# Kernel optimization log

Measured on AMD Instinct MI355X. Metric: run time of the kernel, lower is better.

Reference implementation:

```python
import jax, jax.numpy as jnp
import numpy as np

N = 50000   # nodes
E = 800000  # edges (avg degree 16)
D = 128     # in = hidden = out feats


def setup_inputs() -> dict:
    key = jax.random.key(0)
    ks = jax.random.split(key, 9)
    x = jax.random.normal(ks[0], (N, D), dtype=jnp.float32)
    edge_index = jax.random.randint(ks[1], (2, E), 0, N, dtype=jnp.int64)
    s = 1.0 / np.sqrt(D)
    # SAGEConv layer 0 (128 -> 128): lin_l (aggregated neighbors, with bias), lin_r (root, no bias)
    Wl0 = jax.random.uniform(ks[2], (D, D), jnp.float32, -s, s)
    Wr0 = jax.random.uniform(ks[3], (D, D), jnp.float32, -s, s)
    b0 = jax.random.uniform(ks[4], (D,), jnp.float32, -s, s)
    # SAGEConv layer 1 (128 -> 128)
    Wl1 = jax.random.uniform(ks[5], (D, D), jnp.float32, -s, s)
    Wr1 = jax.random.uniform(ks[6], (D, D), jnp.float32, -s, s)
    b1 = jax.random.uniform(ks[7], (D,), jnp.float32, -s, s)
    return {"x": x, "edge_index": edge_index,
            "Wl0": Wl0, "Wr0": Wr0, "b0": b0,
            "Wl1": Wl1, "Wr1": Wr1, "b1": b1}


def _sage_conv(x, src, dst, Wl, Wr, b):
    # mean aggregation of neighbor messages x[src] into dst nodes
    msgs = x[src]                                                    # [E, D]
    summed = jax.ops.segment_sum(msgs, dst, num_segments=N)         # [N, D]
    deg = jax.ops.segment_sum(jnp.ones((src.shape[0], 1), x.dtype), dst,
                              num_segments=N)                       # [N, 1]
    agg = summed / jnp.maximum(deg, 1.0)
    # out = lin_l(agg) + lin_r(x); only lin_l has bias (PyG default)
    return agg @ Wl.T + b + x @ Wr.T


def reference(x, edge_index, Wl0, Wr0, b0, Wl1, Wr1, b1):
    src, dst = edge_index[0], edge_index[1]
    h = jax.nn.relu(_sage_conv(x, src, dst, Wl0, Wr0, b0))
    out = _sage_conv(h, src, dst, Wl1, Wr1, b1)  # no ReLU on last layer
    return out
```

## Files before the change

### kernel.cpp

```cpp
#include <hip/hip_runtime.h>


#define D 128
#define NBITS 7
#define BNODES 128
#define GA 64
typedef unsigned short u16;
typedef unsigned u32;
typedef short bf16x8 __attribute__((ext_vector_type(8)));
typedef float f32x4 __attribute__((ext_vector_type(4)));

__device__ __forceinline__ u16 f2bf(float f) {
    union { float f; unsigned u; } x;
    x.f = f;
    unsigned r = x.u + 0x7FFF + ((x.u >> 16) & 1);
    return (u16)(r >> 16);
}
__device__ __forceinline__ float bf2f(u16 b) {
    union { unsigned u; float f; } x;
    x.u = ((unsigned)b) << 16;
    return x.f;
}


__global__ __launch_bounds__(1024) void bucket_hist(const int* __restrict__ dst,
                                                    int* __restrict__ Gcounts,
                                                    int E, int NB, int chunk) {
    __shared__ int cnt[512];
    for (int i = threadIdx.x; i < NB; i += 1024) cnt[i] = 0;
    __syncthreads();
    int base = blockIdx.x * chunk;
    int end = base + chunk; if (end > E) end = E;
    for (int e = base + threadIdx.x; e < end; e += 1024)
        atomicAdd(&cnt[dst[e] >> NBITS], 1);
    __syncthreads();
    for (int b = threadIdx.x; b < NB; b += 1024)
        Gcounts[b * GA + blockIdx.x] = cnt[b];
}

__global__ __launch_bounds__(1024) void scan1_kernel(const int* __restrict__ in,
                                                     int* __restrict__ excl,
                                                     int* __restrict__ totals, int n) {
    int chunk = blockIdx.x;
    int i = chunk * 1024 + threadIdx.x;
    int v = (i < n) ? in[i] : 0;
    int lane = threadIdx.x & 63;
    int wid = threadIdx.x >> 6;
    int s = v;
    #pragma unroll
    for (int off = 1; off < 64; off <<= 1) {
        int t = __shfl_up(s, off);
        if (lane >= off) s += t;
    }
    __shared__ int wsum[16];
    if (lane == 63) wsum[wid] = s;
    __syncthreads();
    if (wid == 0) {
        int ws = (lane < 16) ? wsum[lane] : 0;
        #pragma unroll
        for (int off = 1; off < 16; off <<= 1) {
            int t = __shfl_up(ws, off);
            if (lane >= off) ws += t;
        }
        if (lane < 16) wsum[lane] = ws;
    }
    __syncthreads();
    int wave_off = (wid > 0) ? wsum[wid - 1] : 0;
    int incl = s + wave_off;
    if (i < n) excl[i] = incl - v;
    if (threadIdx.x == 1023) totals[chunk] = incl;
}

__global__ __launch_bounds__(1024) void scan_add(int* __restrict__ Sc,
                                                 const int* __restrict__ totals, int n) {
    int chunk = blockIdx.x;
    int i = chunk * 1024 + threadIdx.x;
    int off = 0;
    for (int j = 0; j < chunk; ++j) off += totals[j];
    if (i < n) Sc[i] += off;
}

__global__ __launch_bounds__(1024) void bucket_scatter(const int* __restrict__ src,
                                                       const int* __restrict__ dst,
                                                       const int* __restrict__ Sc,
                                                       u32* __restrict__ Ebuck,
                                                       int E, int NB, int chunk) {
    __shared__ int cur[512];
    for (int b = threadIdx.x; b < NB; b += 1024) cur[b] = Sc[b * GA + blockIdx.x];
    __syncthreads();
    int base = blockIdx.x * chunk;
    int end = base + chunk; if (end > E) end = E;
    for (int e = base + threadIdx.x; e < end; e += 1024) {
        int d = dst[e];
        int b = d >> NBITS;
        int pos = atomicAdd(&cur[b], 1);
        Ebuck[pos] = ((u32)(d & (BNODES - 1)) << 16) | (u32)src[e];
    }
}

__global__ __launch_bounds__(256) void bucket_sort_csr(u32* __restrict__ Ebuck,
                                                       const int* __restrict__ Sc,
                                                       int* __restrict__ row_ptr,
                                                       int E, int N, int NB) {
    __shared__ int hist[BNODES], excl[BNODES], cur[BNODES];
    __shared__ u16 sorted[8192];
    int b = blockIdx.x;
    int start = Sc[b * GA];
    int endv = (b + 1 < NB) ? Sc[(b + 1) * GA] : E;
    int cnt = endv - start;
    if (cnt > 8192) cnt = 8192;
    for (int i = threadIdx.x; i < BNODES; i += 256) hist[i] = 0;
    __syncthreads();
    for (int i = threadIdx.x; i < cnt; i += 256)
        atomicAdd(&hist[Ebuck[start + i] >> 16], 1);
    __syncthreads();
    if (threadIdx.x == 0) {
        int run = 0;
        for (int i = 0; i < BNODES; ++i) { excl[i] = run; run += hist[i]; }
    }
    __syncthreads();
    for (int i = threadIdx.x; i < BNODES; i += 256) {
        cur[i] = excl[i];
        int g = b * BNODES + i;
        if (g <= N) row_ptr[g] = start + excl[i];
    }
    __syncthreads();
    for (int i = threadIdx.x; i < cnt; i += 256) {
        u32 r = Ebuck[start + i];
        int pos = atomicAdd(&cur[r >> 16], 1);
        sorted[pos] = (u16)(r & 0xFFFF);
    }
    __syncthreads();
    for (int i = threadIdx.x; i < cnt; i += 256)
        ((int*)Ebuck)[start + i] = (int)sorted[i];
}

__global__ void f32_to_bf16_kernel(const float* __restrict__ in, u16* __restrict__ out, int n4) {
    int i = blockIdx.x * 256 + threadIdx.x;
    if (i < n4) {
        float4 v = *(const float4*)&in[i * 4];
        ushort4 o;
        o.x = f2bf(v.x); o.y = f2bf(v.y); o.z = f2bf(v.z); o.w = f2bf(v.w);
        *(ushort4*)&out[i * 4] = o;
    }
}

__global__ void convert_weights(const float* __restrict__ w0, const float* __restrict__ w1,
                                const float* __restrict__ w2, const float* __restrict__ w3,
                                u16* __restrict__ o0, u16* __restrict__ o1,
                                u16* __restrict__ o2, u16* __restrict__ o3) {
    int i = blockIdx.x * 256 + threadIdx.x;
    const int q = D * D / 4;
    int m = i / q, j = i % q;
    const float* in = (m == 0) ? w0 : (m == 1) ? w1 : (m == 2) ? w2 : w3;
    u16* out = (m == 0) ? o0 : (m == 1) ? o1 : (m == 2) ? o2 : o3;
    float4 v = *(const float4*)&in[j * 4];
    ushort4 o;
    o.x = f2bf(v.x); o.y = f2bf(v.y); o.z = f2bf(v.z); o.w = f2bf(v.w);
    *(ushort4*)&out[j * 4] = o;
}

__global__ __launch_bounds__(256) void aggregate_bf16(const u16* __restrict__ xb,
                                                      const int* __restrict__ row_ptr,
                                                      const int* __restrict__ csr,
                                                      u16* __restrict__ aggb, int n) {
    int node = blockIdx.x * 4 + (threadIdx.x >> 6);
    if (node >= n) return;
    int lane = threadIdx.x & 63;
    int half = lane >> 5;
    int fl = (lane & 31) * 4;
    int begin = row_ptr[node], end = row_ptr[node + 1];
    float a0 = 0.f, a1 = 0.f, a2 = 0.f, a3 = 0.f;
    int j = begin + half;
    for (; j + 2 < end; j += 4) {
        int s0 = csr[j], s1 = csr[j + 2];
        ushort4 v0 = *(const ushort4*)&xb[s0 * D + fl];
        ushort4 v1 = *(const ushort4*)&xb[s1 * D + fl];
        a0 += bf2f(v0.x) + bf2f(v1.x);
        a1 += bf2f(v0.y) + bf2f(v1.y);
        a2 += bf2f(v0.z) + bf2f(v1.z);
        a3 += bf2f(v0.w) + bf2f(v1.w);
    }
    if (j < end) {
        int s0 = csr[j];
        ushort4 v0 = *(const ushort4*)&xb[s0 * D + fl];
        a0 += bf2f(v0.x); a1 += bf2f(v0.y); a2 += bf2f(v0.z); a3 += bf2f(v0.w);
    }
    a0 += __shfl_xor(a0, 32);
    a1 += __shfl_xor(a1, 32);
    a2 += __shfl_xor(a2, 32);
    a3 += __shfl_xor(a3, 32);
    if (half == 0) {
        int d = end - begin;
        if (d < 1) d = 1;
        float inv = 1.0f / (float)d;
        ushort4 o;
        o.x = f2bf(a0 * inv); o.y = f2bf(a1 * inv);
        o.z = f2bf(a2 * inv); o.w = f2bf(a3 * inv);
        *(ushort4*)&aggb[node * D + fl] = o;
    }
}

#define LSTR 136

__global__ __launch_bounds__(256) void gemm_mfma(const u16* __restrict__ Aroot,
                                                 const u16* __restrict__ Wr,
                                                 const u16* __restrict__ Agg,
                                                 const u16* __restrict__ Wl,
                                                 const float* __restrict__ bias,
                                                 void* __restrict__ out,
                                                 int n, int mode) {
    __shared__ __align__(16) u16 Lr[64 * LSTR];
    __shared__ __align__(16) u16 Lg[64 * LSTR];
    const int tid = threadIdx.x;
    const int n0 = blockIdx.x * 64;

    {
        int row = tid >> 4;
        int c = (tid & 15) * 8;
        #pragma unroll
        for (int p = 0; p < 4; ++p) {
            int r = p * 16 + row;
            int g = n0 + r;
            float4 vr = make_float4(0.f, 0.f, 0.f, 0.f);
            float4 vg = make_float4(0.f, 0.f, 0.f, 0.f);
            if (g < n) {
                vr = *(const float4*)&Aroot[g * D + c];
                vg = *(const float4*)&Agg[g * D + c];
            }
            *(float4*)&Lr[r * LSTR + c] = vr;
            *(float4*)&Lg[r * LSTR + c] = vg;
        }
    }

    const int wave = tid >> 6;
    const int lane = tid & 63;
    const int quad = lane >> 4;
    const int l16 = lane & 15;

    bf16x8 wr[2][4], wl[2][4];
    #pragma unroll
    for (int mt = 0; mt < 2; ++mt) {
        int jrow = wave * 32 + mt * 16 + l16;
        #pragma unroll
        for (int kb = 0; kb < 4; ++kb) {
            wr[mt][kb] = *(const bf16x8*)&Wr[jrow * D + kb * 32 + quad * 8];
            wl[mt][kb] = *(const bf16x8*)&Wl[jrow * D + kb * 32 + quad * 8];
        }
    }

    __syncthreads();

    f32x4 acc[4][2];
    #pragma unroll
    for (int it = 0; it < 4; ++it)
        #pragma unroll
        for (int mt = 0; mt < 2; ++mt)
            acc[it][mt] = (f32x4){0.f, 0.f, 0.f, 0.f};

    #pragma unroll
    for (int it = 0; it < 4; ++it) {
        int base = (it * 16 + l16) * LSTR + quad * 8;
        #pragma unroll
        for (int kb = 0; kb < 4; ++kb) {
            bf16x8 bx = *(const bf16x8*)&Lr[base + kb * 32];
            bf16x8 bg = *(const bf16x8*)&Lg[base + kb * 32];
            #pragma unroll
            for (int mt = 0; mt < 2; ++mt) {
                acc[it][mt] = __builtin_amdgcn_mfma_f32_16x16x32_bf16(wr[mt][kb], bx, acc[it][mt], 0, 0, 0);
                acc[it][mt] = __builtin_amdgcn_mfma_f32_16x16x32_bf16(wl[mt][kb], bg, acc[it][mt], 0, 0, 0);
            }
        }
    }

    #pragma unroll
    for (int it = 0; it < 4; ++it) {
        int i = n0 + it * 16 + l16;
        if (i < n) {
            #pragma unroll
            for (int mt = 0; mt < 2; ++mt) {
                int j0 = wave * 32 + mt * 16 + quad * 4;
                float4 bv = *(const float4*)&bias[j0];
                float o0 = acc[it][mt][0] + bv.x;
                float o1 = acc[it][mt][1] + bv.y;
                float o2 = acc[it][mt][2] + bv.z;
                float o3 = acc[it][mt][3] + bv.w;
                if (mode) {
                    o0 = fmaxf(o0, 0.f); o1 = fmaxf(o1, 0.f);
                    o2 = fmaxf(o2, 0.f); o3 = fmaxf(o3, 0.f);
                    ushort4 ob;
                    ob.x = f2bf(o0); ob.y = f2bf(o1); ob.z = f2bf(o2); ob.w = f2bf(o3);
                    *(ushort4*)&((u16*)out)[i * D + j0] = ob;
                } else {
                    float4 of = make_float4(o0, o1, o2, o3);
                    *(float4*)&((float*)out)[i * D + j0] = of;
                }
            }
        }
    }
}


extern "C" void kernel_launch(void* const* d_in, const int* in_sizes, int n_in,
                              void* d_out, int out_size, void* d_ws, size_t ws_size,
                              hipStream_t stream) {
    const float* x = (const float*)d_in[0];
    const int* edge = (const int*)d_in[1];
    const float* Wl0 = (const float*)d_in[2];
    const float* Wr0 = (const float*)d_in[3];
    const float* b0 = (const float*)d_in[4];
    const float* Wl1 = (const float*)d_in[5];
    const float* Wr1 = (const float*)d_in[6];
    const float* b1 = (const float*)d_in[7];

    const int N = in_sizes[0] / D;
    const int E = in_sizes[1] / 2;
    const int* src = edge;
    const int* dst = edge + E;

    char* ws = (char*)d_ws;
    size_t off = 0;
    auto alloc = [&](size_t bytes) {
        char* p = ws + off;
        off += (bytes + 255) & ~(size_t)255;
        return p;
    };
    int* row_ptr = (int*)alloc((size_t)(N + 1) * 4);
    u32* Ebuck = (u32*)alloc((size_t)E * 4);
    u16* xb = (u16*)alloc((size_t)N * D * 2);
    u16* hb = (u16*)alloc((size_t)N * D * 2);
    u16* aggb = (u16*)alloc((size_t)N * D * 2);
    u16* Wl0b = (u16*)alloc((size_t)D * D * 2);
    u16* Wr0b = (u16*)alloc((size_t)D * D * 2);
    u16* Wl1b = (u16*)alloc((size_t)D * D * 2);
    u16* Wr1b = (u16*)alloc((size_t)D * D * 2);
    const int NB = (N + BNODES - 1) / BNODES;
    const int scanN = NB * GA;
    int* Gcounts = (int*)aggb;
    int* Sc = Gcounts + scanN;
    int* totals = Sc + scanN;

    (void)ws_size; (void)n_in; (void)out_size;

    const int chunk = (E + GA - 1) / GA;
    const int scanBlocks = (scanN + 1023) / 1024;

    bucket_hist<<<GA, 1024, 0, stream>>>(dst, Gcounts, E, NB, chunk);
    scan1_kernel<<<scanBlocks, 1024, 0, stream>>>(Gcounts, Sc, totals, scanN);
    scan_add<<<scanBlocks, 1024, 0, stream>>>(Sc, totals, scanN);
    bucket_scatter<<<GA, 1024, 0, stream>>>(src, dst, Sc, Ebuck, E, NB, chunk);
    bucket_sort_csr<<<NB, 256, 0, stream>>>(Ebuck, Sc, row_ptr, E, N, NB);
    const int* csr = (const int*)Ebuck;

    int xQuads = N * D / 4;
    f32_to_bf16_kernel<<<(xQuads + 255) / 256, 256, 0, stream>>>(x, xb, xQuads);
    convert_weights<<<(4 * D * D / 4 + 255) / 256, 256, 0, stream>>>(
        Wl0, Wr0, Wl1, Wr1, Wl0b, Wr0b, Wl1b, Wr1b);

    int aggBlocks = (N + 3) / 4;
    int gemmBlocks = (N + 63) / 64;

    aggregate_bf16<<<aggBlocks, 256, 0, stream>>>(xb, row_ptr, csr, aggb, N);
    gemm_mfma<<<gemmBlocks, 256, 0, stream>>>(xb, Wr0b, aggb, Wl0b, b0, hb, N, 1);
    aggregate_bf16<<<aggBlocks, 256, 0, stream>>>(hb, row_ptr, csr, aggb, N);
    gemm_mfma<<<gemmBlocks, 256, 0, stream>>>(hb, Wr1b, aggb, Wl1b, b1, d_out, N, 0);
}
```

Measured before the change: 228.9 us.

## Shard neighbor aggregation across feature chunks with eight edges per wave

```diff
diff --git a/kernel.cpp b/kernel.cpp
--- a/kernel.cpp
+++ b/kernel.cpp
@@ -5,6 +5,7 @@
 #define NBITS 7
 #define BNODES 128
 #define GA 64
+#define NPG 16
 typedef unsigned short u16;
 typedef unsigned u32;
 typedef short bf16x8 __attribute__((ext_vector_type(8)));
@@ -160,44 +161,48 @@
     *(ushort4*)&out[j * 4] = o;
 }
 
-__global__ __launch_bounds__(256) void aggregate_bf16(const u16* __restrict__ xb,
-                                                      const int* __restrict__ row_ptr,
-                                                      const int* __restrict__ csr,
-                                                      u16* __restrict__ aggb, int n) {
-    int node = blockIdx.x * 4 + (threadIdx.x >> 6);
-    if (node >= n) return;
-    int lane = threadIdx.x & 63;
-    int half = lane >> 5;
-    int fl = (lane & 31) * 4;
-    int begin = row_ptr[node], end = row_ptr[node + 1];
-    float a0 = 0.f, a1 = 0.f, a2 = 0.f, a3 = 0.f;
-    int j = begin + half;
-    for (; j + 2 < end; j += 4) {
-        int s0 = csr[j], s1 = csr[j + 2];
-        ushort4 v0 = *(const ushort4*)&xb[s0 * D + fl];
-        ushort4 v1 = *(const ushort4*)&xb[s1 * D + fl];
-        a0 += bf2f(v0.x) + bf2f(v1.x);
-        a1 += bf2f(v0.y) + bf2f(v1.y);
-        a2 += bf2f(v0.z) + bf2f(v1.z);
-        a3 += bf2f(v0.w) + bf2f(v1.w);
-    }
-    if (j < end) {
-        int s0 = csr[j];
-        ushort4 v0 = *(const ushort4*)&xb[s0 * D + fl];
-        a0 += bf2f(v0.x); a1 += bf2f(v0.y); a2 += bf2f(v0.z); a3 += bf2f(v0.w);
-    }
-    a0 += __shfl_xor(a0, 32);
-    a1 += __shfl_xor(a1, 32);
-    a2 += __shfl_xor(a2, 32);
-    a3 += __shfl_xor(a3, 32);
-    if (half == 0) {
-        int d = end - begin;
-        if (d < 1) d = 1;
-        float inv = 1.0f / (float)d;
-        ushort4 o;
-        o.x = f2bf(a0 * inv); o.y = f2bf(a1 * inv);
-        o.z = f2bf(a2 * inv); o.w = f2bf(a3 * inv);
-        *(ushort4*)&aggb[node * D + fl] = o;
+__global__ __launch_bounds__(256) void aggregate_sharded(const u16* __restrict__ xb,
+                                                         const int* __restrict__ row_ptr,
+                                                         const int* __restrict__ csr,
+                                                         u16* __restrict__ aggb, int n) {
+    const int chunk = blockIdx.x & 7;
+    const int grp = blockIdx.x >> 3;
+    const int wave = threadIdx.x >> 6;
+    const int lane = threadIdx.x & 63;
+    const int g = lane >> 3;
+    const int f = lane & 7;
+    const int cbase = chunk * 16 + f * 2;
+
+    #pragma unroll
+    for (int i = 0; i < NPG / 4; ++i) {
+        int node = grp * NPG + wave * (NPG / 4) + i;
+        if (node >= n) return;
+        int begin = row_ptr[node], end = row_ptr[node + 1];
+        float a0 = 0.f, a1 = 0.f;
+        int j = begin + g;
+        for (; j + 8 < end; j += 16) {
+            int s0 = csr[j], s1 = csr[j + 8];
+            u32 v0 = *(const u32*)&xb[s0 * D + cbase];
+            u32 v1 = *(const u32*)&xb[s1 * D + cbase];
+            a0 += bf2f((u16)(v0 & 0xFFFF)) + bf2f((u16)(v1 & 0xFFFF));
+            a1 += bf2f((u16)(v0 >> 16)) + bf2f((u16)(v1 >> 16));
+        }
+        if (j < end) {
+            int s0 = csr[j];
+            u32 v0 = *(const u32*)&xb[s0 * D + cbase];
+            a0 += bf2f((u16)(v0 & 0xFFFF));
+            a1 += bf2f((u16)(v0 >> 16));
+        }
+        a0 += __shfl_xor(a0, 8);  a1 += __shfl_xor(a1, 8);
+        a0 += __shfl_xor(a0, 16); a1 += __shfl_xor(a1, 16);
+        a0 += __shfl_xor(a0, 32); a1 += __shfl_xor(a1, 32);
+        if (g == 0) {
+            int d = end - begin;
+            if (d < 1) d = 1;
+            float inv = 1.0f / (float)d;
+            u32 o = ((u32)f2bf(a1 * inv) << 16) | (u32)f2bf(a0 * inv);
+            *(u32*)&aggb[node * D + cbase] = o;
+        }
     }
 }
 
@@ -357,11 +362,11 @@
     convert_weights<<<(4 * D * D / 4 + 255) / 256, 256, 0, stream>>>(
         Wl0, Wr0, Wl1, Wr1, Wl0b, Wr0b, Wl1b, Wr1b);
 
-    int aggBlocks = (N + 3) / 4;
+    int aggBlocks = 8 * ((N + NPG - 1) / NPG);
     int gemmBlocks = (N + 63) / 64;
 
-    aggregate_bf16<<<aggBlocks, 256, 0, stream>>>(xb, row_ptr, csr, aggb, N);
+    aggregate_sharded<<<aggBlocks, 256, 0, stream>>>(xb, row_ptr, csr, aggb, N);
     gemm_mfma<<<gemmBlocks, 256, 0, stream>>>(xb, Wr0b, aggb, Wl0b, b0, hb, N, 1);
-    aggregate_bf16<<<aggBlocks, 256, 0, stream>>>(hb, row_ptr, csr, aggb, N);
+    aggregate_sharded<<<aggBlocks, 256, 0, stream>>>(hb, row_ptr, csr, aggb, N);
     gemm_mfma<<<gemmBlocks, 256, 0, stream>>>(hb, Wr1b, aggb, Wl1b, b1, d_out, N, 0);
 }
```

New measurement: 363.6 us. 58.8% more time.
